# Optimization experiments

Measured on AMD Instinct MI355X. Metric: run time of the kernel, lower is better.

Reference implementation:

```python
import jax, jax.numpy as jnp
import numpy as np

H = 2048
K_SRC = (H * H) // 4  # exact nonzero count of mask_src (fixed in setup_inputs)
K_TAR = (H * H) // 4  # exact nonzero count of mask_tar
NBINS = 256


def de_norm(x):
    return jnp.clip((x + 1.0) / 2.0, 0.0, 1.0)


def cal_hist_cdf(vals):
    # vals: [3, K] float in [0, 255]. torch.histc(bins=256, min=0, max=256)
    # has unit-width bins -> bin index = floor(v). Returns cumulative pdf [3, 256].
    idx = jnp.clip(vals.astype(jnp.int32), 0, NBINS - 1)
    flat = (idx + jnp.arange(3, dtype=jnp.int32)[:, None] * NBINS).ravel()
    hist = jnp.bincount(flat, length=3 * NBINS).reshape(3, NBINS).astype(vals.dtype)
    pdf = hist / hist.sum(axis=1, keepdims=True)
    return jnp.cumsum(pdf, axis=1)


def cal_trans(dst_cdf, ref_cdf):
    # Faithful to PSGAN cal_trans(ref=dst_cdf, adj=ref_cdf):
    # table[i] = first j in [1,255] with ref_cdf[j-1] <= dst_cdf[i] <= ref_cdf[j],
    # else i; table[255] = 255. First valid j equals searchsorted-left (clipped).
    i = jnp.arange(NBINS)
    j = jnp.clip(jnp.searchsorted(ref_cdf, dst_cdf, side='left'), 1, NBINS - 1)
    valid = (ref_cdf[j - 1] <= dst_cdf) & (dst_cdf <= ref_cdf[j])
    table = jnp.where(valid, j, i)
    return table.at[NBINS - 1].set(NBINS - 1)


def setup_inputs():
    key = jax.random.key(0)
    k1, k2 = jax.random.split(key)
    rng = np.random.default_rng(0)

    def make_mask(K):
        m = np.zeros(H * H, np.float32)
        m[rng.permutation(H * H)[:K]] = 1.0
        return jnp.asarray(m.reshape(1, 1, H, H))

    return {
        "input_data": jax.random.normal(k1, (1, 3, H, H), jnp.float32),
        "target_data": jax.random.normal(k2, (1, 3, H, H), jnp.float32),
        "mask_src": make_mask(K_SRC),
        "mask_tar": make_mask(K_TAR),
    }


def reference(input_data, target_data, mask_src, mask_tar):
    m_src = mask_src[0, 0]  # [H, H]
    m_tar = mask_tar[0, 0]
    # nonzero() returns row-major (y, x) index pairs, same as torch
    ys, xs = jnp.nonzero(m_src, size=K_SRC)
    yt, xt = jnp.nonzero(m_tar, size=K_TAR)

    inp = de_norm(input_data)[0] * 255.0   # [3, H, H]
    tar = de_norm(target_data)[0] * 255.0
    input_masked = inp * m_src[None]
    target_masked = tar * m_tar[None]

    dst_align = input_masked[:, ys, xs]    # [3, K_SRC]
    ref_align = target_masked[:, yt, xt]   # [3, K_TAR]

    cdf_dst = cal_hist_cdf(dst_align)
    cdf_ref = cal_hist_cdf(ref_align)
    tables = jax.vmap(cal_trans)(cdf_dst, cdf_ref)  # [3, 256]

    # remap: tables[c][int(dst_align[c,k])] (int() truncation, values >= 0)
    bins = jnp.clip(dst_align.astype(jnp.int32), 0, NBINS - 1)
    mapped = jnp.take_along_axis(tables, bins, axis=1).astype(input_masked.dtype)

    # scatter matched values back into the masked input image; detached in torch
    input_match = jax.lax.stop_gradient(input_masked.at[:, ys, xs].set(mapped))
    return jnp.mean(jnp.abs(input_masked - input_match))
```

## Files before the change

kernel.cpp:

```cpp
#include <hip/hip_runtime.h>
#include <hip/hip_bf16.h>

#define HDIM 2048
#define HH (HDIM * HDIM)
#define NBINS 256
#define KCNT 1048576.0f
#define TOTAL_ELEMS 12582912.0

#define FRAC_SCALE 33554432.0f
#define FRAC_INV   (1.0 / 33554432.0)
#define FRAC_MASK  ((1ull << 40) - 1)

#define ROW_U64    1152
#define ROW_BYTES  9216
#define TAIL_BYTES (1536 * sizeof(int) + 768 * sizeof(unsigned long long))
#define ROWS_PER_CHUNK 32

__device__ __forceinline__ float de_norm255(float x) {
    float v = (x + 1.0f) * 0.5f;
    v = fminf(fmaxf(v, 0.0f), 1.0f) * 255.0f;
    return v;
}

__global__ void hist_kernel(const float* __restrict__ inp,
                            const float* __restrict__ tar,
                            const float* __restrict__ msrc,
                            const float* __restrict__ mtar,
                            unsigned long long* __restrict__ parts) {
    __shared__ unsigned long long h64[3 * NBINS];
    __shared__ unsigned long long dummy64[64];
    __shared__ unsigned int       h32[3 * NBINS];
    for (int i = threadIdx.x; i < 3 * NBINS; i += blockDim.x) {
        h64[i] = 0ull;
        h32[i] = 0u;
    }
    if (threadIdx.x < 64) dummy64[threadIdx.x] = 0ull;
    __syncthreads();

    const int lane = threadIdx.x & 63;
    unsigned long long* const dslot = &dummy64[lane];

    int nz[6] = {0, 0, 0, 0, 0, 0};
    int nf[6] = {0, 0, 0, 0, 0, 0};

    const int stride = gridDim.x * blockDim.x;
    const int n4 = HH / 4;
    for (int p4 = blockIdx.x * blockDim.x + threadIdx.x; p4 < n4; p4 += stride) {
        float4 ms4 = ((const float4*)msrc)[p4];
        float4 mt4 = ((const float4*)mtar)[p4];
        float m[4] = {ms4.x, ms4.y, ms4.z, ms4.w};
        float t[4] = {mt4.x, mt4.y, mt4.z, mt4.w};
        #pragma unroll
        for (int c = 0; c < 3; ++c) {
            float4 v4 = ((const float4*)(inp + (size_t)c * HH))[p4];
            float4 w4 = ((const float4*)(tar + (size_t)c * HH))[p4];
            float vv[4] = {v4.x, v4.y, v4.z, v4.w};
            float ww[4] = {w4.x, w4.y, w4.z, w4.w};
            #pragma unroll
            for (int k = 0; k < 4; ++k) {
                {
                    const bool on = (m[k] != 0.0f);
                    float v = de_norm255(vv[k]);
                    int b = (int)v;
                    float frac = v - (float)b;
                    unsigned fx = (unsigned)(frac * FRAC_SCALE);
                    const bool mid = on & (v > 0.0f) & (v < 255.0f);
                    unsigned long long* addr = mid ? &h64[c * NBINS + b] : dslot;
                    atomicAdd(addr, (1ull << 40) | (unsigned long long)fx);
                    nz[c] += (int)(on & (v == 0.0f));
                    nf[c] += (int)(on & (v == 255.0f));
                }
                {
                    const bool on = (t[k] != 0.0f);
                    float w = de_norm255(ww[k]);
                    int b = (int)w;
                    const bool mid = on & (w > 0.0f) & (w < 255.0f);
                    unsigned int* addr = mid ? &h32[c * NBINS + b]
                                             : (unsigned int*)dslot;
                    atomicAdd(addr, 1u);
                    nz[3 + c] += (int)(on & (w == 0.0f));
                    nf[3 + c] += (int)(on & (w == 255.0f));
                }
            }
        }
    }

    #pragma unroll
    for (int j = 0; j < 6; ++j) {
        int a = nz[j], f = nf[j];
        #pragma unroll
        for (int off = 32; off > 0; off >>= 1) {
            a += __shfl_down(a, off, 64);
            f += __shfl_down(f, off, 64);
        }
        if (lane == 0) {
            if (j < 3) {
                if (a) atomicAdd(&h64[j * NBINS + 0],
                                 ((unsigned long long)a) << 40);
                if (f) atomicAdd(&h64[j * NBINS + NBINS - 1],
                                 ((unsigned long long)f) << 40);
            } else {
                if (a) atomicAdd(&h32[(j - 3) * NBINS + 0], (unsigned)a);
                if (f) atomicAdd(&h32[(j - 3) * NBINS + NBINS - 1], (unsigned)f);
            }
        }
    }
    __syncthreads();

    unsigned long long* row64 = parts + (size_t)blockIdx.x * ROW_U64;
    for (int i = threadIdx.x; i < 3 * NBINS; i += blockDim.x)
        row64[i] = h64[i];
    unsigned int* row32 = (unsigned int*)(row64 + 3 * NBINS);
    for (int i = threadIdx.x; i < 3 * NBINS; i += blockDim.x)
        row32[i] = h32[i];
}

__global__ void reduce_kernel(const unsigned long long* __restrict__ parts,
                              int nblk,
                              int* __restrict__ counts,
                              unsigned long long* __restrict__ fracs) {
    const int j = blockIdx.x * blockDim.x + threadIdx.x;
    if (j >= 1536) return;
    int w0 = blockIdx.y * ROWS_PER_CHUNK;
    int w1 = w0 + ROWS_PER_CHUNK;
    if (w1 > nblk) w1 = nblk;
    if (w0 >= w1) return;

    if (j < 768) {
        unsigned long long cnt = 0, fr = 0;
        for (int w = w0; w < w1; ++w) {
            unsigned long long p = parts[(size_t)w * ROW_U64 + j];
            cnt += p >> 40;
            fr  += p & FRAC_MASK;
        }
        if (cnt) atomicAdd(&counts[j], (int)cnt);
        if (fr)  atomicAdd(&fracs[j], fr);
    } else {
        const unsigned int* p32 = (const unsigned int*)parts;
        int cnt = 0;
        const int jj = j - 768;
        for (int w = w0; w < w1; ++w)
            cnt += p32[(size_t)w * (2 * ROW_U64) + 1536 + jj];
        if (cnt) atomicAdd(&counts[768 + jj], cnt);
    }
}

__global__ void final_kernel(const int* __restrict__ counts,
                             const unsigned long long* __restrict__ fracs,
                             float* __restrict__ out) {
    __shared__ float cdf[6][NBINS];
    __shared__ int   lcnt[6 * NBINS];
    __shared__ double red[12];
    const int tid = threadIdx.x;
    lcnt[tid]       = counts[tid];
    lcnt[tid + 768] = counts[tid + 768];
    __syncthreads();

    if (tid < 6) {
        float run = 0.0f;
        for (int i = 0; i < NBINS; ++i) {
            run += (float)lcnt[tid * NBINS + i] * (1.0f / KCNT);
            cdf[tid][i] = run;
        }
    }
    __syncthreads();

    const int c = tid >> 8, b = tid & (NBINS - 1);
    const float d = cdf[c][b];
    const float* r = cdf[3 + c];
    int lo = 0, hi = NBINS;
    while (lo < hi) {
        int mid = (lo + hi) >> 1;
        if (r[mid] < d) lo = mid + 1; else hi = mid;
    }
    int j = lo;
    if (j < 1) j = 1;
    if (j > NBINS - 1) j = NBINS - 1;
    bool valid = (r[j - 1] <= d) && (d <= r[j]);
    int t = valid ? j : b;
    if (b == NBINS - 1) t = NBINS - 1;

    const int n = lcnt[c * NBINS + b];
    const double s = (double)n * (double)b
                   + (double)(long long)fracs[c * NBINS + b] * FRAC_INV;
    double contrib = (t <= b) ? (s - (double)n * (double)t)
                              : ((double)n * (double)t - s);

    #pragma unroll
    for (int off = 32; off > 0; off >>= 1)
        contrib += __shfl_down(contrib, off, 64);
    const int wave = tid >> 6, lane = tid & 63;
    if (lane == 0) red[wave] = contrib;
    __syncthreads();
    if (tid == 0) {
        double tot = 0.0;
        for (int w = 0; w < 12; ++w) tot += red[w];
        out[0] = (float)(tot / TOTAL_ELEMS);
    }
}

extern "C" void kernel_launch(void* const* d_in, const int* in_sizes, int n_in,
                              void* d_out, int out_size, void* d_ws, size_t ws_size,
                              hipStream_t stream) {
    const float* inp  = (const float*)d_in[0];
    const float* tar  = (const float*)d_in[1];
    const float* msrc = (const float*)d_in[2];
    const float* mtar = (const float*)d_in[3];
    float* out = (float*)d_out;

    int nblk = 2048;
    if (ws_size < (size_t)nblk * ROW_BYTES + TAIL_BYTES) {
        size_t avail = ws_size > TAIL_BYTES ? (ws_size - TAIL_BYTES) / ROW_BYTES : 1;
        nblk = avail < 256 ? 256 : (int)avail;
        if (nblk > 2048) nblk = 2048;
    }

    char* ws = (char*)d_ws;
    unsigned long long* parts = (unsigned long long*)ws;
    int*                counts = (int*)(ws + (size_t)nblk * ROW_BYTES);
    unsigned long long* fracs  = (unsigned long long*)(ws + (size_t)nblk * ROW_BYTES
                                                          + 1536 * sizeof(int));

    hipMemsetAsync((void*)counts, 0, TAIL_BYTES, stream);

    const int nchunks = (nblk + ROWS_PER_CHUNK - 1) / ROWS_PER_CHUNK;
    dim3 rgrid(6, nchunks);

    hist_kernel<<<nblk, 256, 0, stream>>>(inp, tar, msrc, mtar, parts);
    reduce_kernel<<<rgrid, 256, 0, stream>>>(parts, nblk, counts, fracs);
    final_kernel<<<1, 3 * NBINS, 0, stream>>>(counts, fracs, out);
}
```

Measured before the change: 55.35 us.

## Software-pipeline histogram loads with fixed 512-block grid and masked-lane skips

Fixes the histogram grid at 512 blocks, so each thread handles exactly 8 iterations. The next iteration's eight float4 loads are issued before the current one is processed, giving register double-buffering. The branchless dummy-slot atomics become branches, so masked-off and saturated pixels skip the LDS atomic entirely; half the pixels are masked out, which cuts atomic traffic. The costs are higher register pressure, fewer blocks, less latency hiding through occupancy, and the loss of the workspace-size fallback.

```diff
diff --git a/kernel.cpp b/kernel.cpp
--- a/kernel.cpp
+++ b/kernel.cpp
@@ -11,6 +11,7 @@
 #define FRAC_INV   (1.0 / 33554432.0)
 #define FRAC_MASK  ((1ull << 40) - 1)
 
+#define NBLK 512
 #define ROW_U64    1152
 #define ROW_BYTES  9216
 #define TAIL_BYTES (1536 * sizeof(int) + 768 * sizeof(unsigned long long))
@@ -22,69 +23,85 @@
     return v;
 }
 
-__global__ void hist_kernel(const float* __restrict__ inp,
-                            const float* __restrict__ tar,
-                            const float* __restrict__ msrc,
-                            const float* __restrict__ mtar,
-                            unsigned long long* __restrict__ parts) {
+__global__ void __launch_bounds__(256) hist_kernel(
+        const float* __restrict__ inp,
+        const float* __restrict__ tar,
+        const float* __restrict__ msrc,
+        const float* __restrict__ mtar,
+        unsigned long long* __restrict__ parts) {
     __shared__ unsigned long long h64[3 * NBINS];
-    __shared__ unsigned long long dummy64[64];
     __shared__ unsigned int       h32[3 * NBINS];
     for (int i = threadIdx.x; i < 3 * NBINS; i += blockDim.x) {
         h64[i] = 0ull;
         h32[i] = 0u;
     }
-    if (threadIdx.x < 64) dummy64[threadIdx.x] = 0ull;
-    __syncthreads();
-
-    const int lane = threadIdx.x & 63;
-    unsigned long long* const dslot = &dummy64[lane];
+    __syncthreads();
 
     int nz[6] = {0, 0, 0, 0, 0, 0};
     int nf[6] = {0, 0, 0, 0, 0, 0};
 
-    const int stride = gridDim.x * blockDim.x;
-    const int n4 = HH / 4;
-    for (int p4 = blockIdx.x * blockDim.x + threadIdx.x; p4 < n4; p4 += stride) {
-        float4 ms4 = ((const float4*)msrc)[p4];
-        float4 mt4 = ((const float4*)mtar)[p4];
-        float m[4] = {ms4.x, ms4.y, ms4.z, ms4.w};
-        float t[4] = {mt4.x, mt4.y, mt4.z, mt4.w};
+    const int stride = NBLK * 256;
+    const int tid0   = blockIdx.x * 256 + threadIdx.x;
+    const float4* msrc4 = (const float4*)msrc;
+    const float4* mtar4 = (const float4*)mtar;
+
+    float4 ms = msrc4[tid0];
+    float4 mt = mtar4[tid0];
+    float4 a0 = ((const float4*)(inp + 0 * (size_t)HH))[tid0];
+    float4 a1 = ((const float4*)(inp + 1 * (size_t)HH))[tid0];
+    float4 a2 = ((const float4*)(inp + 2 * (size_t)HH))[tid0];
+    float4 b0 = ((const float4*)(tar + 0 * (size_t)HH))[tid0];
+    float4 b1 = ((const float4*)(tar + 1 * (size_t)HH))[tid0];
+    float4 b2 = ((const float4*)(tar + 2 * (size_t)HH))[tid0];
+
+    #pragma unroll 1
+    for (int it = 0; it < 8; ++it) {
+        const int pn = tid0 + ((it < 7) ? (it + 1) : it) * stride;
+        float4 ms_n = msrc4[pn];
+        float4 mt_n = mtar4[pn];
+        float4 a0_n = ((const float4*)(inp + 0 * (size_t)HH))[pn];
+        float4 a1_n = ((const float4*)(inp + 1 * (size_t)HH))[pn];
+        float4 a2_n = ((const float4*)(inp + 2 * (size_t)HH))[pn];
+        float4 b0_n = ((const float4*)(tar + 0 * (size_t)HH))[pn];
+        float4 b1_n = ((const float4*)(tar + 1 * (size_t)HH))[pn];
+        float4 b2_n = ((const float4*)(tar + 2 * (size_t)HH))[pn];
+
+        const float m[4] = {ms.x, ms.y, ms.z, ms.w};
+        const float t[4] = {mt.x, mt.y, mt.z, mt.w};
+        const float4 av[3] = {a0, a1, a2};
+        const float4 bv[3] = {b0, b1, b2};
         #pragma unroll
         for (int c = 0; c < 3; ++c) {
-            float4 v4 = ((const float4*)(inp + (size_t)c * HH))[p4];
-            float4 w4 = ((const float4*)(tar + (size_t)c * HH))[p4];
-            float vv[4] = {v4.x, v4.y, v4.z, v4.w};
-            float ww[4] = {w4.x, w4.y, w4.z, w4.w};
+            const float vv[4] = {av[c].x, av[c].y, av[c].z, av[c].w};
+            const float ww[4] = {bv[c].x, bv[c].y, bv[c].z, bv[c].w};
             #pragma unroll
             for (int k = 0; k < 4; ++k) {
-                {
-                    const bool on = (m[k] != 0.0f);
+                if (m[k] != 0.0f) {
                     float v = de_norm255(vv[k]);
-                    int b = (int)v;
-                    float frac = v - (float)b;
-                    unsigned fx = (unsigned)(frac * FRAC_SCALE);
-                    const bool mid = on & (v > 0.0f) & (v < 255.0f);
-                    unsigned long long* addr = mid ? &h64[c * NBINS + b] : dslot;
-                    atomicAdd(addr, (1ull << 40) | (unsigned long long)fx);
-                    nz[c] += (int)(on & (v == 0.0f));
-                    nf[c] += (int)(on & (v == 255.0f));
+                    if (v == 0.0f)        nz[c]++;
+                    else if (v == 255.0f) nf[c]++;
+                    else {
+                        int bb = (int)v;
+                        float frac = v - (float)bb;
+                        unsigned fx = (unsigned)(frac * FRAC_SCALE);
+                        atomicAdd(&h64[c * NBINS + bb],
+                                  (1ull << 40) | (unsigned long long)fx);
+                    }
                 }
-                {
-                    const bool on = (t[k] != 0.0f);
+                if (t[k] != 0.0f) {
                     float w = de_norm255(ww[k]);
-                    int b = (int)w;
-                    const bool mid = on & (w > 0.0f) & (w < 255.0f);
-                    unsigned int* addr = mid ? &h32[c * NBINS + b]
-                                             : (unsigned int*)dslot;
-                    atomicAdd(addr, 1u);
-                    nz[3 + c] += (int)(on & (w == 0.0f));
-                    nf[3 + c] += (int)(on & (w == 255.0f));
+                    if (w == 0.0f)        nz[3 + c]++;
+                    else if (w == 255.0f) nf[3 + c]++;
+                    else atomicAdd(&h32[c * NBINS + (int)w], 1u);
                 }
             }
         }
-    }
-
+        ms = ms_n; mt = mt_n;
+        a0 = a0_n; a1 = a1_n; a2 = a2_n;
+        b0 = b0_n; b1 = b1_n; b2 = b2_n;
+    }
+
+    const int lane = threadIdx.x & 63;
     #pragma unroll
     for (int j = 0; j < 6; ++j) {
         int a = nz[j], f = nf[j];
@@ -208,25 +225,18 @@
     const float* mtar = (const float*)d_in[3];
     float* out = (float*)d_out;
 
-    int nblk = 2048;
-    if (ws_size < (size_t)nblk * ROW_BYTES + TAIL_BYTES) {
-        size_t avail = ws_size > TAIL_BYTES ? (ws_size - TAIL_BYTES) / ROW_BYTES : 1;
-        nblk = avail < 256 ? 256 : (int)avail;
-        if (nblk > 2048) nblk = 2048;
-    }
-
     char* ws = (char*)d_ws;
     unsigned long long* parts = (unsigned long long*)ws;
-    int*                counts = (int*)(ws + (size_t)nblk * ROW_BYTES);
-    unsigned long long* fracs  = (unsigned long long*)(ws + (size_t)nblk * ROW_BYTES
+    int*                counts = (int*)(ws + (size_t)NBLK * ROW_BYTES);
+    unsigned long long* fracs  = (unsigned long long*)(ws + (size_t)NBLK * ROW_BYTES
                                                           + 1536 * sizeof(int));
 
     hipMemsetAsync((void*)counts, 0, TAIL_BYTES, stream);
 
-    const int nchunks = (nblk + ROWS_PER_CHUNK - 1) / ROWS_PER_CHUNK;
+    const int nchunks = (NBLK + ROWS_PER_CHUNK - 1) / ROWS_PER_CHUNK;
     dim3 rgrid(6, nchunks);
 
-    hist_kernel<<<nblk, 256, 0, stream>>>(inp, tar, msrc, mtar, parts);
-    reduce_kernel<<<rgrid, 256, 0, stream>>>(parts, nblk, counts, fracs);
+    hist_kernel<<<NBLK, 256, 0, stream>>>(inp, tar, msrc, mtar, parts);
+    reduce_kernel<<<rgrid, 256, 0, stream>>>(parts, NBLK, counts, fracs);
     final_kernel<<<1, 3 * NBINS, 0, stream>>>(counts, fracs, out);
 }
```

Result: no change. 54.63 us (-1.3%).
